# Kernel optimization log

Measured on AMD Instinct MI355X. Metric: run time of the kernel, lower is better.

The kernel has to match this reference:

```python
import jax, jax.numpy as jnp
import numpy as np

N, HID, K, L, OUT = 325, 64, 2, 2, 1


def _supports(adj):
    # dual random walk: transposed random-walk matrices D^-1 W (as in original DCRNN)
    S1 = (adj / adj.sum(1, keepdims=True)).T
    adjT = adj.T
    S2 = (adjT / adjT.sum(1, keepdims=True)).T
    return (S1, S2)


def _gconv(x, h, W, b, supports):
    # x: [B, N*in_dim], h: [B, N*HID]
    B = x.shape[0]
    xh = jnp.concatenate([x.reshape(B, N, -1), h.reshape(B, N, -1)], -1)  # [B,N,C]
    C = xh.shape[-1]
    x0 = xh.transpose(1, 2, 0).reshape(N, C * B)  # [N, C*B]
    mats = [x0]
    for S in supports:
        x1 = S @ x0
        mats.append(x1)
        xk2, xk1 = x0, x1
        for _ in range(2, K + 1):
            x2 = 2.0 * (S @ xk1) - xk2
            mats.append(x2)
            xk2, xk1 = xk1, x2
    M = len(mats)  # 2*K + 1 = 5
    xs = jnp.stack(mats, 0).reshape(M, N, C, B).transpose(3, 1, 2, 0).reshape(B * N, C * M)
    return xs @ W + b


def _cell(x, h, Wg, bg, Wc, bc, supports):
    B = x.shape[0]
    val = jax.nn.sigmoid(_gconv(x, h, Wg, bg, supports).reshape(B, N, 2 * HID))
    r, u = jnp.split(val, 2, axis=-1)
    r = r.reshape(B, N * HID)
    u = u.reshape(B, N * HID)
    c = jnp.tanh(_gconv(x, r * h, Wc, bc, supports).reshape(B, N * HID))
    return u * h + (1.0 - u) * c


def setup_inputs() -> dict:
    key = jax.random.key(0)
    ks = jax.random.split(key, 14)
    B, H1 = 64, 13
    return {
        "inputs": jax.random.normal(ks[0], (H1, B, N, 1), jnp.float32),
        "init_state": jax.random.normal(ks[1], (L, B, N * HID), jnp.float32) * 0.1,
        "adj_mx": jax.random.uniform(ks[2], (N, N), jnp.float32, 0.01, 1.0),
        "Wg0": jax.random.normal(ks[3], ((1 + HID) * (2 * K + 1), 2 * HID), jnp.float32) * 0.05,
        "bg0": jnp.ones((2 * HID,), jnp.float32),
        "Wc0": jax.random.normal(ks[4], ((1 + HID) * (2 * K + 1), HID), jnp.float32) * 0.05,
        "bc0": jnp.zeros((HID,), jnp.float32),
        "Wg1": jax.random.normal(ks[5], ((2 * HID) * (2 * K + 1), 2 * HID), jnp.float32) * 0.05,
        "bg1": jnp.ones((2 * HID,), jnp.float32),
        "Wc1": jax.random.normal(ks[6], ((2 * HID) * (2 * K + 1), HID), jnp.float32) * 0.05,
        "bc1": jnp.zeros((HID,), jnp.float32),
        "W_fc": jax.random.normal(ks[7], (HID, OUT), jnp.float32) * 0.1,
        "b_fc": jnp.zeros((OUT,), jnp.float32),
        "teaching_force_ratio": 1,
    }


def reference(inputs, init_state, adj_mx, Wg0, bg0, Wc0, bc0, Wg1, bg1, Wc1, bc1, W_fc, b_fc, teaching_force_ratio):
    H1, B = inputs.shape[0], inputs.shape[1]
    inp = inputs.reshape(H1, B, -1)
    supports = _supports(adj_mx)
    params = ((Wg0, bg0, Wc0, bc0), (Wg1, bg1, Wc1, bc1))

    def step(carry, x_t):
        cur, state = carry
        layer_in = cur
        hs = []
        for l in range(L):
            h_new = _cell(layer_in, state[l], params[l][0], params[l][1], params[l][2], params[l][3], supports)
            layer_in = h_new
            hs.append(h_new)
        state = jnp.stack(hs, 0)
        out = (h_new.reshape(-1, HID) @ W_fc + b_fc).reshape(B, N * OUT)
        # teaching_force_ratio == 1 -> teacher forcing every step (deterministic)
        return (x_t, state), out

    (_, _), outs = jax.lax.scan(step, (inp[0], init_state), inp[1:])
    zero0 = jnp.zeros((1, B, N * OUT), outs.dtype)  # outputs[0] left as zeros, matching torch code
    return jnp.concatenate([zero0, outs], 0)
```

## Files before the change

### kernel.cpp

```cpp
#include <hip/hip_runtime.h>
#include <math.h>

#define NN    325
#define BB    64
#define TT    12
#define NODE  4096
#define KD    352
#define NPADR 384
#define XP    360
#define OBP   72
#define KP0   352
#define KP1   640
#define SB2   512

typedef unsigned short ushort;
typedef __attribute__((ext_vector_type(8))) short short8v;
typedef __attribute__((ext_vector_type(4))) short short4v;
typedef __attribute__((ext_vector_type(4))) float float4v;

static __device__ __forceinline__ ushort f2bf(float f){
  unsigned u = __builtin_bit_cast(unsigned, f);
  u += 0x7fffu + ((u >> 16) & 1u);
  return (ushort)(u >> 16);
}

__global__ void k_sums(const float* __restrict__ adj, float* __restrict__ rs,
                       float* __restrict__ cs){
  __shared__ float red[8];
  int j = blockIdx.x;
  int tid = threadIdx.x, gq = tid >> 6;
  float rv = 0.f, cv = 0.f;
  for (int k = tid; k < NN; k += 256){
    rv += adj[j*NN + k];
    cv += adj[k*NN + j];
  }
  #pragma unroll
  for (int o = 32; o > 0; o >>= 1){
    rv += __shfl_down(rv, o);
    cv += __shfl_down(cv, o);
  }
  if ((tid & 63) == 0){ red[gq] = rv; red[4 + gq] = cv; }
  __syncthreads();
  if (tid == 0){
    rs[j] = red[0]+red[1]+red[2]+red[3];
    cs[j] = red[4]+red[5]+red[6]+red[7];
  }
}

__global__ void k_setup2(const float* __restrict__ adj, const float* __restrict__ rs,
                         const float* __restrict__ cs, const float* __restrict__ inp,
                         const float* __restrict__ init,
                         const float* __restrict__ Wg0, const float* __restrict__ Wc0,
                         const float* __restrict__ Wg1, const float* __restrict__ Wc1,
                         float* __restrict__ Sfp, ushort* __restrict__ Scomb,
                         ushort* __restrict__ Wg0t, ushort* __restrict__ Wc0t,
                         ushort* __restrict__ Wg1t, ushort* __restrict__ Wc1t,
                         float* __restrict__ h0, float* __restrict__ h1,
                         ushort* __restrict__ matsL0, ushort* __restrict__ matsL1){
  int bx = blockIdx.x, t = threadIdx.x;
  if (bx < NN){
    int n = bx, b = t & 63, cq = t >> 6;
    #pragma unroll
    for (int ii = 0; ii < 16; ++ii){
      int c = cq*16 + ii;
      float h0v = init[(size_t)(b*NN + n)*64 + c];
      float h1v = init[(size_t)BB*NN*64 + (size_t)(b*NN + n)*64 + c];
      h0[(size_t)n*NODE + c*64 + b] = h0v;
      h1[(size_t)n*NODE + c*64 + b] = h1v;
      matsL0[((size_t)(1 + c)*NN + n)*64 + b]  = f2bf(h0v);
      matsL1[((size_t)c*NN + n)*64 + b]        = f2bf(h0v);
      matsL1[((size_t)(64 + c)*NN + n)*64 + b] = f2bf(h1v);
    }
    if (t < 64)
      matsL0[(size_t)n*64 + t] = f2bf(inp[(size_t)t*NN + n]);
  }
  for (int idx = bx*256 + t; idx < 2*NN*NN; idx += SB2*256){
    int s = idx / (NN*NN), rem = idx - s*(NN*NN);
    int i = rem / NN, j = rem - i*NN;
    float v = s ? adj[i*NN + j]/cs[j] : adj[j*NN + i]/rs[j];
    Sfp[idx] = v;
    Scomb[(size_t)(2*s)*NPADR*KD + (size_t)i*KD + j] = f2bf(v);
  }
  {
    const float* Ws[4] = { Wg0, Wc0, Wg1, Wc1 };
    ushort* Wts[4]     = { Wg0t, Wc0t, Wg1t, Wc1t };
    const int Cs[4] = { 65, 65, 128, 128 };
    const int Os[4] = { 128, 64, 128, 64 };
    const int Kp[4] = { KP0, KP0, KP1, KP1 };
    for (int q = 0; q < 4; ++q){
      int total = Os[q]*Kp[q];
      for (int idx = bx*256 + t; idx < total; idx += SB2*256){
        int o = idx / Kp[q], k = idx - o*Kp[q];
        int m = k / Cs[q], c = k - m*Cs[q];
        Wts[q][idx] = f2bf(m < 5 ? Ws[q][(c*5 + m)*Os[q] + o] : 0.f);
      }
    }
  }
}

__global__ __launch_bounds__(256) void k_s2(const float* __restrict__ Sfp,
                                            ushort* __restrict__ Scomb){
  __shared__ ushort X[64][XP];
  int jt = blockIdx.x, rh2 = blockIdx.y, s = blockIdx.z;
  int t = threadIdx.x, w = t >> 6, r = t & 15, g = (t >> 4) & 3;
  const float* S = Sfp + (size_t)s*NN*NN;
  for (int idx = t; idx < KD*8; idx += 256){
    int k = idx >> 3, j0 = (idx & 7)*8;
    #pragma unroll
    for (int i = 0; i < 8; ++i){
      int j = j0 + i, col = jt*64 + j;
      float v = (k < NN && col < NN) ? S[(size_t)k*NN + col] : 0.f;
      X[j][k] = f2bf(v);
    }
  }
  __syncthreads();
  const ushort* A = Scomb + (size_t)(2*s)*NPADR*KD + (size_t)(rh2*192)*KD;
  float4v acc[3][4];
  #pragma unroll
  for (int i = 0; i < 3; ++i)
    #pragma unroll
    for (int q = 0; q < 4; ++q) acc[i][q] = (float4v){0.f,0.f,0.f,0.f};
  for (int kc = 0; kc < KD/32; ++kc){
    short8v a[3], bbv[4];
    #pragma unroll
    for (int mt = 0; mt < 3; ++mt)
      a[mt] = *(const short8v*)&A[(size_t)((w*3 + mt)*16 + r)*KD + kc*32 + g*8];
    #pragma unroll
    for (int nt = 0; nt < 4; ++nt)
      bbv[nt] = *(const short8v*)&X[nt*16 + r][kc*32 + g*8];
    #pragma unroll
    for (int mt = 0; mt < 3; ++mt)
      #pragma unroll
      for (int nt = 0; nt < 4; ++nt)
        acc[mt][nt] = __builtin_amdgcn_mfma_f32_16x16x32_bf16(a[mt], bbv[nt], acc[mt][nt], 0, 0, 0);
  }
  ushort* dst = Scomb + (size_t)(2*s + 1)*NPADR*KD;
  #pragma unroll
  for (int mt = 0; mt < 3; ++mt){
    int node0 = rh2*192 + (w*3 + mt)*16 + g*4;
    #pragma unroll
    for (int nt = 0; nt < 4; ++nt){
      int col = nt*16 + r, jg = jt*64 + col;
      #pragma unroll
      for (int i = 0; i < 4; ++i){
        int n = node0 + i;
        if (n < NN && jg < NN)
          dst[(size_t)n*KD + jg] = f2bf(2.f*acc[mt][nt][i] - (n == jg ? 1.f : 0.f));
      }
    }
  }
}

struct Seg {
  const ushort* sm;
  const float*  sf;
  ushort* dm;
  int C, cs0, cd0;
};
struct DiffA {
  const ushort* Sc;
  Seg seg[3];
  int e0, e1, nch;
};

__global__ __launch_bounds__(256, 3) void k_diffN(DiffA da){
  __shared__ ushort X[64][XP];
  ushort (*OB)[OBP] = (ushort (*)[OBP])&X[0][0];
  int lin = blockIdx.x;
  int cu = (lin >> 6)*8 + (lin & 7);
  if (cu >= da.nch) return;
  int sub = (lin >> 3) & 7;
  const int y = sub >> 2, m = sub & 3;
  Seg sg; int u;
  if (cu < da.e0){ sg = da.seg[0]; u = cu; }
  else if (cu < da.e1){ sg = da.seg[1]; u = cu - da.e0; }
  else { sg = da.seg[2]; u = cu - da.e1; }
  int t = threadIdx.x, w = t >> 6;
  int r = t & 15, g = (t >> 4) & 3;

  if (sg.sm){
    const ushort* src = sg.sm + (size_t)(sg.cs0 + u)*NN*64;
    int nb = t >> 3, b0 = (t & 7)*8;
    int swz = (t & 3) << 3;
    const short8v vz = {0,0,0,0,0,0,0,0};
    short8v v[11];
    #pragma unroll
    for (int j = 0; j < 11; ++j){
      int n = j*32 + nb;
      v[j] = (n < NN) ? *(const short8v*)&src[(size_t)n*64 + b0] : vz;
    }
    #pragma unroll
    for (int j = 0; j < 11; ++j){
      int col = (j*32 + nb) ^ swz;
      #pragma unroll
      for (int i = 0; i < 8; ++i) X[b0 + i][col] = (ushort)v[j][i];
    }
  } else {
    for (int j = 0; j < 22; ++j){
      int idx = j*256 + t;
      int b = idx / 88, n4 = (idx - b*88)*4;
      int swz = ((b >> 3) & 3) << 3;
      ushort us[4];
      #pragma unroll
      for (int i = 0; i < 4; ++i)
        us[i] = (n4 + i < NN) ? f2bf(sg.sf[(size_t)b*NN + n4 + i]) : (ushort)0;
      short4v pk; pk[0]=(short)us[0]; pk[1]=(short)us[1]; pk[2]=(short)us[2]; pk[3]=(short)us[3];
      *(short4v*)&X[b][n4 ^ swz] = pk;
      #pragma unroll
      for (int i = 0; i < 4; ++i)
        if (n4 + i < NN) sg.dm[(size_t)(n4 + i)*64 + b] = us[i];
    }
  }
  __syncthreads();

  const ushort* S = da.Sc + ((size_t)m*NPADR + (size_t)y*192)*KD;
  int swr[4];
  #pragma unroll
  for (int nt = 0; nt < 4; ++nt)
    swr[nt] = ((nt*2 + (r >> 3)) & 3) << 3;
  float4v acc[3][4];
  #pragma unroll
  for (int i = 0; i < 3; ++i)
    #pragma unroll
    for (int q = 0; q < 4; ++q) acc[i][q] = (float4v){0.f,0.f,0.f,0.f};
  for (int kc = 0; kc < KD/32; ++kc){
    short8v a[3], bbv[4];
    #pragma unroll
    for (int mt = 0; mt < 3; ++mt)
      a[mt] = *(const short8v*)&S[(size_t)((w*3 + mt)*16 + r)*KD + kc*32 + g*8];
    #pragma unroll
    for (int nt = 0; nt < 4; ++nt)
      bbv[nt] = *(const short8v*)&X[nt*16 + r][(kc*32 + g*8) ^ swr[nt]];
    #pragma unroll
    for (int mt = 0; mt < 3; ++mt)
      #pragma unroll
      for (int nt = 0; nt < 4; ++nt)
        acc[mt][nt] = __builtin_amdgcn_mfma_f32_16x16x32_bf16(a[mt], bbv[nt], acc[mt][nt], 0, 0, 0);
  }

  __syncthreads();
  #pragma unroll
  for (int mt = 0; mt < 3; ++mt){
    int lr0 = (w*3 + mt)*16 + g*4;
    #pragma unroll
    for (int nt = 0; nt < 4; ++nt){
      int col = nt*16 + r;
      #pragma unroll
      for (int i = 0; i < 4; ++i)
        OB[lr0 + i][col] = f2bf(acc[mt][nt][i]);
    }
  }
  __syncthreads();
  {
    ushort* dst = sg.dm + (size_t)((1 + m)*sg.C + sg.cd0 + u)*NN*64;
    int n0 = y*192;
    int lr = t >> 3, q = (t & 7)*8;
    #pragma unroll
    for (int it = 0; it < 6; ++it){
      int row = it*32 + lr;
      int n = n0 + row;
      if (n < NN)
        *(short8v*)&dst[(size_t)n*64 + q] = *(short8v*)&OB[row][q];
    }
  }
}

struct WgD {
  const ushort* mats; const ushort* Wt; const float* bias;
  float* h; float* uu;
  ushort* dstA; ushort* dstB;
  const float* Wfc; const float* bfc; float* outp;
  const float* xnext; ushort* xdst;
  int KPAD; int MODE;
};

template<int KPAD>
static __device__ __forceinline__ void wg_body(
    const WgD& d, int n, int oy, ushort (*XT)[XP], float* fcbuf)
{
  constexpr int NST = (KPAD > 352) ? 2 : 1;
  constexpr int KH  = (KPAD > 352) ? 320 : KPAD;
  constexpr int NCH = KH/32;
  int t = threadIdx.x, w = t >> 6;
  int r = t & 15, g = (t >> 4) & 3;
  const bool fc = (d.MODE == 1) && (d.outp != nullptr);
  if (fc && t < 64) fcbuf[t] = 0.f;

  float4v acc[4];
  #pragma unroll
  for (int nt = 0; nt < 4; ++nt) acc[nt] = (float4v){0.f,0.f,0.f,0.f};

  int kk0 = t >> 3, b0 = (t & 7)*8;
  int swz = (t & 3) << 3;
  int swr[4];
  #pragma unroll
  for (int nt = 0; nt < 4; ++nt)
    swr[nt] = ((nt*2 + (r >> 3)) & 3) << 3;
  #pragma unroll
  for (int st = 0; st < NST; ++st){
    int kbase = st*KH;
    if (st) __syncthreads();
    short8v v[NCH];
    #pragma unroll
    for (int j = 0; j < NCH; ++j)
      v[j] = *(const short8v*)&d.mats[((size_t)(kbase + j*32 + kk0)*NN + n)*64 + b0];
    #pragma unroll
    for (int j = 0; j < NCH; ++j){
      int col = (j*32 + kk0) ^ swz;
      #pragma unroll
      for (int i = 0; i < 8; ++i) XT[b0 + i][col] = (ushort)v[j][i];
    }
    __syncthreads();
    for (int kc = 0; kc < NCH; ++kc){
      short8v a0 = *(const short8v*)&d.Wt[(size_t)(oy*64 + w*16 + r)*KPAD + kbase + kc*32 + g*8];
      short8v bbv[4];
      #pragma unroll
      for (int nt = 0; nt < 4; ++nt)
        bbv[nt] = *(const short8v*)&XT[nt*16 + r][(kc*32 + g*8) ^ swr[nt]];
      #pragma unroll
      for (int nt = 0; nt < 4; ++nt)
        acc[nt] = __builtin_amdgcn_mfma_f32_16x16x32_bf16(a0, bbv[nt], acc[nt], 0, 0, 0);
    }
  }

  __syncthreads();
  #pragma unroll
  for (int nt = 0; nt < 4; ++nt){
    int b2 = nt*16 + r;
    float p = 0.f;
    #pragma unroll
    for (int i = 0; i < 4; ++i){
      int o = w*16 + g*4 + i;
      float vv = acc[nt][i] + d.bias[oy*64 + o];
      if (d.MODE == 0){
        float sg = 1.f/(1.f + expf(-vv));
        if (oy == 0) XT[o][b2] = f2bf(sg * d.h[(size_t)n*NODE + o*64 + b2]);
        else         d.uu[(size_t)n*NODE + o*64 + b2] = sg;
      } else {
        float cv = tanhf(vv);
        size_t idx = (size_t)n*NODE + o*64 + b2;
        float uv = d.uu[idx];
        float hn = uv*d.h[idx] + (1.f - uv)*cv;
        d.h[idx] = hn;
        XT[o][b2] = f2bf(hn);
        if (fc) p += hn * d.Wfc[o];
      }
    }
    if (fc) atomicAdd(&fcbuf[b2], p);
  }
  __syncthreads();
  if (d.MODE == 1 || oy == 0){
    int o = t >> 2, q = (t & 3)*16;
    short8v v0 = *(short8v*)&XT[o][q];
    short8v v1 = *(short8v*)&XT[o][q + 8];
    ushort* dl = d.dstA + ((size_t)o*NN + n)*64 + q;
    *(short8v*)&dl[0] = v0;
    *(short8v*)&dl[8] = v1;
    if (d.dstB){
      ushort* dl2 = d.dstB + ((size_t)o*NN + n)*64 + q;
      *(short8v*)&dl2[0] = v0;
      *(short8v*)&dl2[8] = v1;
    }
  }
  if (d.MODE == 1){
    if (d.xnext && t < 64)
      d.xdst[(size_t)n*64 + t] = f2bf(d.xnext[(size_t)t*NN + n]);
    if (fc && t < 64)
      d.outp[(size_t)t*NN + n] = fcbuf[t] + d.bfc[0];
  }
}

__global__ __launch_bounds__(256) void k_wg2(WgD d0, int n0, WgD d1){
  __shared__ ushort XT[64][XP];
  __shared__ float fcbuf[64];
  const bool first = (blockIdx.x < (unsigned)n0);
  WgD d = first ? d0 : d1;
  int n = first ? blockIdx.x : blockIdx.x - n0;
  int oy = blockIdx.y;
  if (d.MODE == 1 && oy) return;
  if (d.KPAD == 352) wg_body<352>(d, n, oy, XT, fcbuf);
  else               wg_body<640>(d, n, oy, XT, fcbuf);
}

extern "C" void kernel_launch(void* const* d_in, const int* in_sizes, int n_in,
                              void* d_out, int out_size, void* d_ws, size_t ws_size,
                              hipStream_t stream){
  const float* inp  = (const float*)d_in[0];
  const float* init = (const float*)d_in[1];
  const float* adj  = (const float*)d_in[2];
  const float* Wg0  = (const float*)d_in[3];
  const float* bg0  = (const float*)d_in[4];
  const float* Wc0  = (const float*)d_in[5];
  const float* bc0  = (const float*)d_in[6];
  const float* Wg1  = (const float*)d_in[7];
  const float* bg1  = (const float*)d_in[8];
  const float* Wc1  = (const float*)d_in[9];
  const float* bc1  = (const float*)d_in[10];
  const float* Wfc  = (const float*)d_in[11];
  const float* bfc  = (const float*)d_in[12];
  (void)in_sizes; (void)n_in; (void)out_size; (void)ws_size;

  char* p = (char*)d_ws;
  auto alloc = [&](size_t bytes) -> void* {
    void* q = (void*)p; p += (bytes + 255) & ~(size_t)255; return q;
  };
  ushort* Scomb  = (ushort*)alloc((size_t)4*NPADR*KD*2);
  float*  Sfp    = (float*)alloc((size_t)2*NN*NN*4);
  ushort* Wg0t   = (ushort*)alloc((size_t)128*KP0*2);
  ushort* Wc0t   = (ushort*)alloc((size_t)64*KP0*2);
  ushort* Wg1t   = (ushort*)alloc((size_t)128*KP1*2);
  ushort* Wc1t   = (ushort*)alloc((size_t)64*KP1*2);
  float*  rs     = (float*)alloc(512*4);
  float*  cs     = (float*)alloc(512*4);
  float*  h0     = (float*)alloc((size_t)NN*NODE*4);
  float*  h1     = (float*)alloc((size_t)NN*NODE*4);
  float*  uu0    = (float*)alloc((size_t)NN*NODE*4);
  float*  uu1    = (float*)alloc((size_t)NN*NODE*4);
  ushort* matsL0 = (ushort*)alloc((size_t)KP0*NN*64*2);
  ushort* matsL1 = (ushort*)alloc((size_t)KP1*NN*64*2);
  float* out = (float*)d_out;

  hipMemsetAsync(out, 0, (size_t)BB*NN*4, stream);
  hipMemsetAsync(matsL0 + (size_t)325*NN*64, 0, (size_t)(KP0 - 325)*NN*64*2, stream);
  hipMemsetAsync(Scomb, 0, (size_t)4*NPADR*KD*2, stream);

  k_sums<<<NN, 256, 0, stream>>>(adj, rs, cs);
  k_setup2<<<SB2, 256, 0, stream>>>(adj, rs, cs, inp, init, Wg0, Wc0, Wg1, Wc1,
                                    Sfp, Scomb, Wg0t, Wc0t, Wg1t, Wc1t,
                                    h0, h1, matsL0, matsL1);
  k_s2<<<dim3(6, 2, 2), 256, 0, stream>>>(Sfp, Scomb);

  Seg segL0g  = { matsL0, nullptr, matsL0, 65, 0, 0 };
  Seg segL0c  = { matsL0, nullptr, matsL0, 65, 1, 1 };
  Seg segL1h1 = { matsL1, nullptr, matsL1, 128, 64, 64 };
  Seg segL1h0 = { matsL1, nullptr, matsL1, 128, 0, 0 };

  auto diffGrid = [](int nch){ return ((nch + 7)/8)*64; };

  { DiffA da = { Scomb, { segL0g, segL0g, segL0g }, 65, 65, 65 };
    k_diffN<<<diffGrid(65), 256, 0, stream>>>(da); }

  WgD wg_g0 = { matsL0, Wg0t, bg0, h0, uu0, matsL0 + (size_t)1*NN*64, nullptr,
                nullptr, nullptr, nullptr, nullptr, nullptr, KP0, 0 };
  WgD wg_c0 = { matsL0, Wc0t, bc0, h0, uu0, matsL0 + (size_t)1*NN*64, matsL1,
                nullptr, nullptr, nullptr, nullptr, nullptr, KP0, 1 };
  WgD wg_g1 = { matsL1, Wg1t, bg1, h1, uu1, matsL1 + (size_t)64*NN*64, nullptr,
                nullptr, nullptr, nullptr, nullptr, nullptr, KP1, 0 };

  k_wg2<<<dim3(NN, 2), 256, 0, stream>>>(wg_g0, NN, wg_g0);

  for (int t = 0; t < TT; ++t){
    { DiffA da = { Scomb, { segL0c, segL1h1, segL0c }, 64, 128, 128 };
      k_diffN<<<diffGrid(128), 256, 0, stream>>>(da); }
    k_wg2<<<dim3(NN, 1), 256, 0, stream>>>(wg_c0, NN, wg_c0);
    { Seg segX = { nullptr, inp + (size_t)(t + 1)*BB*NN, matsL0, 65, 0, 0 };
      DiffA da = { Scomb, { segL1h0, segL0c, segX }, 64, 128, 129 };
      k_diffN<<<diffGrid(129), 256, 0, stream>>>(da); }
    k_wg2<<<dim3(NN, 2), 256, 0, stream>>>(wg_g1, NN, wg_g1);
    { DiffA da = { Scomb, { segL1h1, segL1h1, segL1h1 }, 64, 64, 64 };
      k_diffN<<<diffGrid(64), 256, 0, stream>>>(da); }
    WgD wg_c1 = { matsL1, Wc1t, bc1, h1, uu1, matsL1 + (size_t)64*NN*64, nullptr,
                  Wfc, bfc, out + (size_t)(t + 1)*BB*NN,
                  (t + 1 < TT) ? inp + (size_t)(t + 1)*BB*NN : nullptr, matsL0,
                  KP1, 1 };
    if (t < TT - 1)
      k_wg2<<<dim3(2*NN, 2), 256, 0, stream>>>(wg_c1, NN, wg_g0);
    else
      k_wg2<<<dim3(NN, 1), 256, 0, stream>>>(wg_c1, NN, wg_c1);
  }
}
```

Measured before the change: 1.676 ms.

## Split diffusion K-loop into two LDS chunks to raise occupancy

```diff
diff --git a/kernel.cpp b/kernel.cpp
--- a/kernel.cpp
+++ b/kernel.cpp
@@ -8,6 +8,9 @@
 #define KD    352
 #define NPADR 384
 #define XP    360
+#define XP2   200
+#define XW0   192
+#define XW1   160
 #define OBP   72
 #define KP0   352
 #define KP1   640
@@ -163,8 +166,8 @@
   int e0, e1, nch;
 };
 
-__global__ __launch_bounds__(256, 3) void k_diffN(DiffA da){
-  __shared__ ushort X[64][XP];
+__global__ __launch_bounds__(256, 5) void k_diffN(DiffA da){
+  __shared__ ushort X[64][XP2];
   ushort (*OB)[OBP] = (ushort (*)[OBP])&X[0][0];
   int lin = blockIdx.x;
   int cu = (lin >> 6)*8 + (lin & 7);
@@ -178,90 +181,110 @@
   int t = threadIdx.x, w = t >> 6;
   int r = t & 15, g = (t >> 4) & 3;
 
-  if (sg.sm){
-    const ushort* src = sg.sm + (size_t)(sg.cs0 + u)*NN*64;
-    int nb = t >> 3, b0 = (t & 7)*8;
-    int swz = (t & 3) << 3;
-    const short8v vz = {0,0,0,0,0,0,0,0};
-    short8v v[11];
-    #pragma unroll
-    for (int j = 0; j < 11; ++j){
-      int n = j*32 + nb;
-      v[j] = (n < NN) ? *(const short8v*)&src[(size_t)n*64 + b0] : vz;
-    }
-    #pragma unroll
-    for (int j = 0; j < 11; ++j){
-      int col = (j*32 + nb) ^ swz;
-      #pragma unroll
-      for (int i = 0; i < 8; ++i) X[b0 + i][col] = (ushort)v[j][i];
-    }
-  } else {
-    for (int j = 0; j < 22; ++j){
-      int idx = j*256 + t;
-      int b = idx / 88, n4 = (idx - b*88)*4;
-      int swz = ((b >> 3) & 3) << 3;
-      ushort us[4];
-      #pragma unroll
-      for (int i = 0; i < 4; ++i)
-        us[i] = (n4 + i < NN) ? f2bf(sg.sf[(size_t)b*NN + n4 + i]) : (ushort)0;
-      short4v pk; pk[0]=(short)us[0]; pk[1]=(short)us[1]; pk[2]=(short)us[2]; pk[3]=(short)us[3];
-      *(short4v*)&X[b][n4 ^ swz] = pk;
-      #pragma unroll
-      for (int i = 0; i < 4; ++i)
-        if (n4 + i < NN) sg.dm[(size_t)(n4 + i)*64 + b] = us[i];
-    }
-  }
+  const ushort* S = da.Sc + ((size_t)m*NPADR + (size_t)y*192)*KD;
+  float4v acc[3][4];
+  #pragma unroll
+  for (int i = 0; i < 3; ++i)
+    #pragma unroll
+    for (int q = 0; q < 4; ++q) acc[i][q] = (float4v){0.f,0.f,0.f,0.f};
+
+  int swr[4];
+  #pragma unroll
+  for (int nt = 0; nt < 4; ++nt)
+    swr[nt] = (((nt*16 + r) >> 3) & 7) << 3;
+
+  #pragma unroll
+  for (int ch = 0; ch < 2; ++ch){
+    const int koff = ch ? XW0 : 0;
+    const int NKC  = ch ? (XW1/32) : (XW0/32);
+    if (ch) __syncthreads();
+    if (sg.sm){
+      const ushort* src = sg.sm + (size_t)(sg.cs0 + u)*NN*64;
+      int nb = t >> 3, b0 = (t & 7)*8;
+      int s3 = (t & 7) << 3;
+      const short8v vz = {0,0,0,0,0,0,0,0};
+      short8v v[6];
+      #pragma unroll
+      for (int j = 0; j < 6; ++j){
+        if (j >= NKC) break;
+        int n = koff + j*32 + nb;
+        v[j] = (n < NN) ? *(const short8v*)&src[(size_t)n*64 + b0] : vz;
+      }
+      #pragma unroll
+      for (int j = 0; j < 6; ++j){
+        if (j >= NKC) break;
+        int col = (j*32 + nb) ^ s3;
+        #pragma unroll
+        for (int i = 0; i < 8; ++i) X[b0 + i][col] = (ushort)v[j][i];
+      }
+    } else {
+      const int W4 = ch ? (XW1/4) : (XW0/4);
+      const int NG = 64*W4;
+      for (int idx = t; idx < NG; idx += 256){
+        int b = idx / W4, n4 = (idx - b*W4)*4;
+        int s3 = ((b >> 3) & 7) << 3;
+        ushort us[4];
+        #pragma unroll
+        for (int i = 0; i < 4; ++i){
+          int n = koff + n4 + i;
+          us[i] = (n < NN) ? f2bf(sg.sf[(size_t)b*NN + n]) : (ushort)0;
+        }
+        short4v pk; pk[0]=(short)us[0]; pk[1]=(short)us[1]; pk[2]=(short)us[2]; pk[3]=(short)us[3];
+        *(short4v*)&X[b][n4 ^ s3] = pk;
+        #pragma unroll
+        for (int i = 0; i < 4; ++i){
+          int n = koff + n4 + i;
+          if (n < NN) sg.dm[(size_t)n*64 + b] = us[i];
+        }
+      }
+    }
+    __syncthreads();
+    for (int kc = 0; kc < NKC; ++kc){
+      short8v a[3], bbv[4];
+      #pragma unroll
+      for (int mt = 0; mt < 3; ++mt)
+        a[mt] = *(const short8v*)&S[(size_t)((w*3 + mt)*16 + r)*KD + koff + kc*32 + g*8];
+      #pragma unroll
+      for (int nt = 0; nt < 4; ++nt)
+        bbv[nt] = *(const short8v*)&X[nt*16 + r][(kc*32 + g*8) ^ swr[nt]];
+      #pragma unroll
+      for (int mt = 0; mt < 3; ++mt)
+        #pragma unroll
+        for (int nt = 0; nt < 4; ++nt)
+          acc[mt][nt] = __builtin_amdgcn_mfma_f32_16x16x32_bf16(a[mt], bbv[nt], acc[mt][nt], 0, 0, 0);
+    }
+  }
+
   __syncthreads();
-
-  const ushort* S = da.Sc + ((size_t)m*NPADR + (size_t)y*192)*KD;
-  int swr[4];
-  #pragma unroll
-  for (int nt = 0; nt < 4; ++nt)
-    swr[nt] = ((nt*2 + (r >> 3)) & 3) << 3;
-  float4v acc[3][4];
-  #pragma unroll
-  for (int i = 0; i < 3; ++i)
-    #pragma unroll
-    for (int q = 0; q < 4; ++q) acc[i][q] = (float4v){0.f,0.f,0.f,0.f};
-  for (int kc = 0; kc < KD/32; ++kc){
-    short8v a[3], bbv[4];
-    #pragma unroll
-    for (int mt = 0; mt < 3; ++mt)
-      a[mt] = *(const short8v*)&S[(size_t)((w*3 + mt)*16 + r)*KD + kc*32 + g*8];
-    #pragma unroll
-    for (int nt = 0; nt < 4; ++nt)
-      bbv[nt] = *(const short8v*)&X[nt*16 + r][(kc*32 + g*8) ^ swr[nt]];
-    #pragma unroll
-    for (int mt = 0; mt < 3; ++mt)
-      #pragma unroll
-      for (int nt = 0; nt < 4; ++nt)
-        acc[mt][nt] = __builtin_amdgcn_mfma_f32_16x16x32_bf16(a[mt], bbv[nt], acc[mt][nt], 0, 0, 0);
-  }
-
-  __syncthreads();
-  #pragma unroll
-  for (int mt = 0; mt < 3; ++mt){
-    int lr0 = (w*3 + mt)*16 + g*4;
-    #pragma unroll
-    for (int nt = 0; nt < 4; ++nt){
-      int col = nt*16 + r;
-      #pragma unroll
-      for (int i = 0; i < 4; ++i)
-        OB[lr0 + i][col] = f2bf(acc[mt][nt][i]);
-    }
-  }
-  __syncthreads();
-  {
-    ushort* dst = sg.dm + (size_t)((1 + m)*sg.C + sg.cd0 + u)*NN*64;
-    int n0 = y*192;
-    int lr = t >> 3, q = (t & 7)*8;
-    #pragma unroll
-    for (int it = 0; it < 6; ++it){
-      int row = it*32 + lr;
-      int n = n0 + row;
-      if (n < NN)
-        *(short8v*)&dst[(size_t)n*64 + q] = *(short8v*)&OB[row][q];
-    }
+  ushort* dst = sg.dm + (size_t)((1 + m)*sg.C + sg.cd0 + u)*NN*64;
+  int n0 = y*192;
+  #pragma unroll
+  for (int half = 0; half < 2; ++half){
+    if ((w >> 1) == half){
+      #pragma unroll
+      for (int mt = 0; mt < 3; ++mt){
+        int lr0 = (w*3 + mt)*16 + g*4 - half*96;
+        #pragma unroll
+        for (int nt = 0; nt < 4; ++nt){
+          int col = nt*16 + r;
+          #pragma unroll
+          for (int i = 0; i < 4; ++i)
+            OB[lr0 + i][col] = f2bf(acc[mt][nt][i]);
+        }
+      }
+    }
+    __syncthreads();
+    {
+      int lr = t >> 3, q = (t & 7)*8;
+      #pragma unroll
+      for (int it = 0; it < 3; ++it){
+        int row = it*32 + lr;
+        int n = n0 + half*96 + row;
+        if (n < NN)
+          *(short8v*)&dst[(size_t)n*64 + q] = *(short8v*)&OB[row][q];
+      }
+    }
+    if (half == 0) __syncthreads();
   }
 }
 
```

Measured after the change: 1.965 ms. +17.2%, slower.

## Skew layer pipeline so layer-0 and layer-1 cells share fused launches

Applied to the files above, without the earlier changes.

```diff
diff --git a/kernel.cpp b/kernel.cpp
--- a/kernel.cpp
+++ b/kernel.cpp
@@ -154,8 +154,8 @@
 struct Seg {
   const ushort* sm;
   const float*  sf;
-  ushort* dm;
-  int C, cs0, cd0;
+  ushort* dm;  int C,  cs0, cd0;
+  ushort* dm2; int C2, cd2;
 };
 struct DiffA {
   const ushort* Sc;
@@ -253,14 +253,19 @@
   __syncthreads();
   {
     ushort* dst = sg.dm + (size_t)((1 + m)*sg.C + sg.cd0 + u)*NN*64;
+    ushort* dst2 = sg.dm2 ? sg.dm2 + (size_t)((1 + m)*sg.C2 + sg.cd2 + u)*NN*64
+                          : nullptr;
     int n0 = y*192;
     int lr = t >> 3, q = (t & 7)*8;
     #pragma unroll
     for (int it = 0; it < 6; ++it){
       int row = it*32 + lr;
       int n = n0 + row;
-      if (n < NN)
-        *(short8v*)&dst[(size_t)n*64 + q] = *(short8v*)&OB[row][q];
+      if (n < NN){
+        short8v vv = *(short8v*)&OB[row][q];
+        *(short8v*)&dst[(size_t)n*64 + q] = vv;
+        if (dst2) *(short8v*)&dst2[(size_t)n*64 + q] = vv;
+      }
     }
   }
 }
@@ -270,7 +275,6 @@
   float* h; float* uu;
   ushort* dstA; ushort* dstB;
   const float* Wfc; const float* bfc; float* outp;
-  const float* xnext; ushort* xdst;
   int KPAD; int MODE;
 };
 
@@ -362,12 +366,8 @@
       *(short8v*)&dl2[8] = v1;
     }
   }
-  if (d.MODE == 1){
-    if (d.xnext && t < 64)
-      d.xdst[(size_t)n*64 + t] = f2bf(d.xnext[(size_t)t*NN + n]);
-    if (fc && t < 64)
-      d.outp[(size_t)t*NN + n] = fcbuf[t] + d.bfc[0];
-  }
+  if (fc && t < 64)
+    d.outp[(size_t)t*NN + n] = fcbuf[t] + d.bfc[0];
 }
 
 __global__ __launch_bounds__(256) void k_wg2(WgD d0, int n0, WgD d1){
@@ -430,41 +430,51 @@
                                     h0, h1, matsL0, matsL1);
   k_s2<<<dim3(6, 2, 2), 256, 0, stream>>>(Sfp, Scomb);
 
-  Seg segL0g  = { matsL0, nullptr, matsL0, 65, 0, 0 };
-  Seg segL0c  = { matsL0, nullptr, matsL0, 65, 1, 1 };
-  Seg segL1h1 = { matsL1, nullptr, matsL1, 128, 64, 64 };
-  Seg segL1h0 = { matsL1, nullptr, matsL1, 128, 0, 0 };
-
   auto diffGrid = [](int nch){ return ((nch + 7)/8)*64; };
 
-  { DiffA da = { Scomb, { segL0g, segL0g, segL0g }, 65, 65, 65 };
-    k_diffN<<<diffGrid(65), 256, 0, stream>>>(da); }
+  Seg segH0d = { matsL0, nullptr, matsL0, 65, 1, 1, matsL1, 128, 0 };
+  Seg segH1  = { matsL1, nullptr, matsL1, 128, 64, 64, nullptr, 0, 0 };
+  Seg segRh0 = { matsL0, nullptr, matsL0, 65, 1, 1, nullptr, 0, 0 };
+  Seg segRh1 = { matsL1, nullptr, matsL1, 128, 64, 64, nullptr, 0, 0 };
 
   WgD wg_g0 = { matsL0, Wg0t, bg0, h0, uu0, matsL0 + (size_t)1*NN*64, nullptr,
-                nullptr, nullptr, nullptr, nullptr, nullptr, KP0, 0 };
+                nullptr, nullptr, nullptr, KP0, 0 };
   WgD wg_c0 = { matsL0, Wc0t, bc0, h0, uu0, matsL0 + (size_t)1*NN*64, matsL1,
-                nullptr, nullptr, nullptr, nullptr, nullptr, KP0, 1 };
+                nullptr, nullptr, nullptr, KP0, 1 };
   WgD wg_g1 = { matsL1, Wg1t, bg1, h1, uu1, matsL1 + (size_t)64*NN*64, nullptr,
-                nullptr, nullptr, nullptr, nullptr, nullptr, KP1, 0 };
-
-  k_wg2<<<dim3(NN, 2), 256, 0, stream>>>(wg_g0, NN, wg_g0);
-
-  for (int t = 0; t < TT; ++t){
-    { DiffA da = { Scomb, { segL0c, segL1h1, segL0c }, 64, 128, 128 };
-      k_diffN<<<diffGrid(128), 256, 0, stream>>>(da); }
-    k_wg2<<<dim3(NN, 1), 256, 0, stream>>>(wg_c0, NN, wg_c0);
-    { Seg segX = { nullptr, inp + (size_t)(t + 1)*BB*NN, matsL0, 65, 0, 0 };
-      DiffA da = { Scomb, { segL1h0, segL0c, segX }, 64, 128, 129 };
-      k_diffN<<<diffGrid(129), 256, 0, stream>>>(da); }
-    k_wg2<<<dim3(NN, 2), 256, 0, stream>>>(wg_g1, NN, wg_g1);
-    { DiffA da = { Scomb, { segL1h1, segL1h1, segL1h1 }, 64, 64, 64 };
-      k_diffN<<<diffGrid(64), 256, 0, stream>>>(da); }
+                nullptr, nullptr, nullptr, KP1, 0 };
+
+  for (int t = 0; t <= TT; ++t){
+    if (t < TT){
+      Seg segX = { nullptr, inp + (size_t)t*BB*NN, matsL0, 65, 0, 0, nullptr, 0, 0 };
+      DiffA da = { Scomb, { segH0d, segH1, segX }, 64, 128, 129 };
+      k_diffN<<<diffGrid(129), 256, 0, stream>>>(da);
+    } else {
+      DiffA da = { Scomb, { segH0d, segH1, segH1 }, 64, 128, 128 };
+      k_diffN<<<diffGrid(128), 256, 0, stream>>>(da);
+    }
+    if (t == 0)
+      k_wg2<<<dim3(NN, 2), 256, 0, stream>>>(wg_g0, NN, wg_g0);
+    else if (t < TT)
+      k_wg2<<<dim3(2*NN, 2), 256, 0, stream>>>(wg_g0, NN, wg_g1);
+    else
+      k_wg2<<<dim3(NN, 2), 256, 0, stream>>>(wg_g1, NN, wg_g1);
+    if (t == 0){
+      DiffA da = { Scomb, { segRh0, segRh0, segRh0 }, 64, 64, 64 };
+      k_diffN<<<diffGrid(64), 256, 0, stream>>>(da);
+    } else if (t < TT){
+      DiffA da = { Scomb, { segRh0, segRh1, segRh1 }, 64, 128, 128 };
+      k_diffN<<<diffGrid(128), 256, 0, stream>>>(da);
+    } else {
+      DiffA da = { Scomb, { segRh1, segRh1, segRh1 }, 64, 64, 64 };
+      k_diffN<<<diffGrid(64), 256, 0, stream>>>(da);
+    }
     WgD wg_c1 = { matsL1, Wc1t, bc1, h1, uu1, matsL1 + (size_t)64*NN*64, nullptr,
-                  Wfc, bfc, out + (size_t)(t + 1)*BB*NN,
-                  (t + 1 < TT) ? inp + (size_t)(t + 1)*BB*NN : nullptr, matsL0,
-                  KP1, 1 };
-    if (t < TT - 1)
-      k_wg2<<<dim3(2*NN, 2), 256, 0, stream>>>(wg_c1, NN, wg_g0);
+                  Wfc, bfc, out + (size_t)t*BB*NN, KP1, 1 };
+    if (t == 0)
+      k_wg2<<<dim3(NN, 1), 256, 0, stream>>>(wg_c0, NN, wg_c0);
+    else if (t < TT)
+      k_wg2<<<dim3(2*NN, 1), 256, 0, stream>>>(wg_c0, NN, wg_c1);
     else
       k_wg2<<<dim3(NN, 1), 256, 0, stream>>>(wg_c1, NN, wg_c1);
   }
```

Result: faster. 1.481 ms (-11.6%).
